# Performance work log

Measured on AMD Instinct MI355X. Metric: run time of the kernel, lower is better.

Reference implementation:

```python
import jax, jax.numpy as jnp
import numpy as np

EPS = 1e-5

def spmm(rows, cols, vals, x, n_out):
    # COO sparse [n_out, n_in] @ x [n_in, d] -> [n_out, d]
    return jax.ops.segment_sum(vals[:, None] * x[cols], rows, num_segments=n_out)

def layernorm(x, g, b):
    mu = jnp.mean(x, axis=-1, keepdims=True)
    var = jnp.var(x, axis=-1, keepdims=True)
    return (x - mu) * jax.lax.rsqrt(var + EPS) * g + b

def setup_inputs() -> dict:
    key = jax.random.key(0)
    ks = jax.random.split(key, 32)
    N, D = 100000, 512
    N0, N1, N2 = 131072, 32768, 8192
    E_s0, E_s1 = 262144, 65536
    E_f0, E_f1 = 1048576, 262144
    s = 1.0 / np.sqrt(D)
    inp = {
        'x': jax.random.normal(ks[0], (N, D), jnp.float32),
        'hist0': jax.random.normal(ks[1], (N, D), jnp.float32),
        'hist1': jax.random.normal(ks[2], (N, D), jnp.float32),
        'w0': jax.random.normal(ks[3], (D, D), jnp.float32) * s,
        'b0': jax.random.normal(ks[4], (D,), jnp.float32) * s,
        'g0': jnp.ones((D,), jnp.float32),
        'beta0': jnp.zeros((D,), jnp.float32),
        'w1': jax.random.normal(ks[5], (D, D), jnp.float32) * s,
        'b1': jax.random.normal(ks[6], (D,), jnp.float32) * s,
        'sadj0_vals': jax.random.uniform(ks[7], (E_s0,), jnp.float32),
        'sadj1_vals': jax.random.uniform(ks[8], (E_s1,), jnp.float32),
        'fadj0_vals': jax.random.uniform(ks[9], (E_f0,), jnp.float32),
        'fadj1_vals': jax.random.uniform(ks[10], (E_f1,), jnp.float32),
        'sid0': jax.random.randint(ks[11], (N0,), 0, N),
        'sid1': jax.random.randint(ks[12], (N1,), 0, N),
        'sid2': jax.random.randint(ks[13], (N2,), 0, N),
        'fid0': jax.random.randint(ks[14], (N0,), 0, N),
        'fid1': jax.random.randint(ks[15], (N1,), 0, N),
        'sadj0_rows': jax.random.randint(ks[16], (E_s0,), 0, N1),
        'sadj0_cols': jax.random.randint(ks[17], (E_s0,), 0, N0),
        'sadj1_rows': jax.random.randint(ks[18], (E_s1,), 0, N2),
        'sadj1_cols': jax.random.randint(ks[19], (E_s1,), 0, N1),
        'fadj0_rows': jax.random.randint(ks[20], (E_f0,), 0, N1),
        'fadj0_cols': jax.random.randint(ks[21], (E_f0,), 0, N0),
        'fadj1_rows': jax.random.randint(ks[22], (E_f1,), 0, N2),
        'fadj1_cols': jax.random.randint(ks[23], (E_f1,), 0, N1),
    }
    return inp

def reference(x, hist0, hist1, w0, b0, g0, beta0, w1, b1,
              sadj0_vals, sadj1_vals, fadj0_vals, fadj1_vals,
              sid0, sid1, sid2, fid0, fid1,
              sadj0_rows, sadj0_cols, sadj1_rows, sadj1_cols,
              fadj0_rows, fadj0_cols, fadj1_rows, fadj1_cols):
    N1 = sid1.shape[0]
    N2 = sid2.shape[0]
    sg = jax.lax.stop_gradient
    # layer 0
    h = x[sid0]                                   # [N0, D]
    h = h - sg(hist0[sid0])                        # variance-reduction correction
    full = sg(spmm(fadj0_rows, fadj0_cols, fadj0_vals, hist0[fid0], N1))
    h = spmm(sadj0_rows, sadj0_cols, sadj0_vals, h, N1) + full  # [N1, D]
    h = h @ w0.T + b0
    h = jax.nn.relu(layernorm(h, g0, beta0))
    # layer 1 (last: no norm/relu)
    h = h - sg(hist1[sid1])
    full = sg(spmm(fadj1_rows, fadj1_cols, fadj1_vals, hist1[fid1], N2))
    h = spmm(sadj1_rows, sadj1_cols, sadj1_vals, h, N2) + full  # [N2, D]
    h = h @ w1.T + b1
    return jax.nn.log_softmax(h, axis=-1)
```

## Files before the change

### kernel.cpp

```cpp
#include <hip/hip_runtime.h>

#define D 512
#define NTAB 100000

typedef __bf16 bf16x8 __attribute__((ext_vector_type(8)));
typedef float f32x4 __attribute__((ext_vector_type(4)));
typedef float f32x2 __attribute__((ext_vector_type(2)));

__device__ __forceinline__ unsigned f2bf(float f){
  union { float f; unsigned u; } v; v.f = f;
  unsigned r = v.u + 0x7fffu + ((v.u >> 16) & 1u);
  return r >> 16;
}
__device__ __forceinline__ float bf2f(unsigned h){
  union { unsigned u; float f; } v; v.u = h << 16; return v.f;
}
__device__ __forceinline__ uint2 enc_fp8x8(f32x4 v0, f32x4 v1){
  int lo = __builtin_amdgcn_cvt_pk_fp8_f32(v0[0], v0[1], 0, false);
  lo     = __builtin_amdgcn_cvt_pk_fp8_f32(v0[2], v0[3], lo, true);
  int hi = __builtin_amdgcn_cvt_pk_fp8_f32(v1[0], v1[1], 0, false);
  hi     = __builtin_amdgcn_cvt_pk_fp8_f32(v1[2], v1[3], hi, true);
  return make_uint2((unsigned)lo, (unsigned)hi);
}

#define PER8 (NTAB*D/8)

#define MA_NS   6400
#define MA_GRID (MA_NS*9 + 512)

__global__ __launch_bounds__(256) void k_megaA(
    const int* __restrict__ s0r, int nS0,
    const int* __restrict__ f0r, int nF0, int* __restrict__ cnt0,
    const int* __restrict__ s1r, int nS1, int* __restrict__ cnt_s1,
    const int* __restrict__ f1r, int nF1, int* __restrict__ cnt_f1,
    const float* __restrict__ x, const float* __restrict__ hist0, const float* __restrict__ hist1,
    unsigned char* __restrict__ TD,
    unsigned short* __restrict__ H1b,
    const float* __restrict__ w0, const float* __restrict__ w1,
    unsigned short* __restrict__ w0b, unsigned short* __restrict__ w1b)
{
  int b = blockIdx.x, t = threadIdx.x;
  if (b < MA_NS*9){
    int sb = b / 9, r = b % 9;
    if (r == 0){
      int i = sb*256 + t;
      if (i < nS0){ atomicAdd(&cnt0[s0r[i]], 1); return; }
      i -= nS0;
      if (i < nF0){ atomicAdd(&cnt0[f0r[i]], 1); return; }
      i -= nF0;
      if (i < nS1){ atomicAdd(&cnt_s1[s1r[i]], 1); return; }
      i -= nS1;
      atomicAdd(&cnt_f1[f1r[i]], 1);
      return;
    }
    if (r < 5){
      int ci = (sb*4 + (r-1))*256 + t;
      if (ci >= PER8) return;
      const f32x4* px = (const f32x4*)(x     + (size_t)ci*8);
      const f32x4* ph = (const f32x4*)(hist0 + (size_t)ci*8);
      f32x4 x0 = __builtin_nontemporal_load(px);
      f32x4 x1 = __builtin_nontemporal_load(px+1);
      f32x4 h0 = __builtin_nontemporal_load(ph);
      f32x4 h1 = __builtin_nontemporal_load(ph+1);
      *(uint2*)(TD + (size_t)ci*8)                    = enc_fp8x8(x0 - h0, x1 - h1);
      *(uint2*)(TD + (size_t)NTAB*D + (size_t)ci*8)   = enc_fp8x8(h0, h1);
      return;
    }
    {
      int ci = (sb*4 + (r-5))*256 + t;
      if (ci >= PER8) return;
      const f32x4* p = (const f32x4*)(hist1 + (size_t)ci*8);
      f32x4 v0 = __builtin_nontemporal_load(p);
      f32x4 v1 = __builtin_nontemporal_load(p+1);
      uint4 o;
      o.x = f2bf(v0[0]) | (f2bf(v0[1])<<16);
      o.y = f2bf(v0[2]) | (f2bf(v0[3])<<16);
      o.z = f2bf(v1[0]) | (f2bf(v1[1])<<16);
      o.w = f2bf(v1[2]) | (f2bf(v1[3])<<16);
      *(uint4*)(H1b + (size_t)ci*8) = o;
      return;
    }
  } else {
    int i = (b - MA_NS*9)*256 + t;
    const float* src = (i < 65536) ? w0 : w1;
    unsigned short* dst = (i < 65536) ? w0b : w1b;
    int ii = (i < 65536) ? i : i - 65536;
    f32x4 v = *(const f32x4*)(src + (size_t)ii*4);
    ushort4 o;
    o.x = (unsigned short)f2bf(v[0]); o.y = (unsigned short)f2bf(v[1]);
    o.z = (unsigned short)f2bf(v[2]); o.w = (unsigned short)f2bf(v[3]);
    *(ushort4*)(dst + (size_t)ii*4) = o;
  }
}

__global__ __launch_bounds__(1024) void k_exscan3(
    const int* c0, int* r0, int n0,
    const int* c1, int* r1, int n1,
    const int* c2, int* r2, int n2)
{
  __shared__ int part[1024];
  const int* cnt; int* rp; int n;
  switch (blockIdx.x){
    case 0: cnt=c0; rp=r0; n=n0; break;
    case 1: cnt=c1; rp=r1; n=n1; break;
    default: cnt=c2; rp=r2; n=n2; break;
  }
  int t = threadIdx.x;
  int chunk = n >> 10;
  int base = t*chunk;
  int s = 0;
  for (int i=0;i<chunk;i++) s += cnt[base+i];
  part[t] = s; __syncthreads();
  for (int off=1; off<1024; off<<=1){
    int v = (t>=off) ? part[t-off] : 0;
    __syncthreads();
    part[t] += v;
    __syncthreads();
  }
  int run = (t==0) ? 0 : part[t-1];
  for (int i=0;i<chunk;i++){ rp[base+i] = run; run += cnt[base+i]; }
  if (t == 1023) rp[n] = run;
}

__global__ __launch_bounds__(256) void k_fill(
    const int* __restrict__ s0r, const int* __restrict__ s0c, const float* __restrict__ s0v, int nS0,
    const int* __restrict__ f0r, const int* __restrict__ f0c, const float* __restrict__ f0v, int nF0,
    const int* __restrict__ sid0, const int* __restrict__ fid0,
    const int* __restrict__ rp0, int* __restrict__ fill0, int2* __restrict__ bce0,
    const int* __restrict__ s1r, const int* __restrict__ s1c, const float* __restrict__ s1v, int nS1,
    const int* __restrict__ rp_s1, int* __restrict__ fill_s1, int2* __restrict__ bce_s1,
    const int* __restrict__ f1r, const int* __restrict__ f1c, const float* __restrict__ f1v,
    const int* __restrict__ fid1,
    const int* __restrict__ rp_f1, int* __restrict__ fill_f1, int2* __restrict__ bce_f1)
{
  int i = blockIdx.x*256 + threadIdx.x;
  if (i < nS0){
    int rr = s0r[i];
    int c  = sid0[s0c[i]];
    int p = atomicAdd(&fill0[rr], 1);
    bce0[rp0[rr] + p] = make_int2(c, __float_as_int(s0v[i]));
    return;
  }
  i -= nS0;
  if (i < nF0){
    int rr = f0r[i];
    int c  = NTAB + fid0[f0c[i]];
    int p = atomicAdd(&fill0[rr], 1);
    bce0[rp0[rr] + p] = make_int2(c, __float_as_int(f0v[i]));
    return;
  }
  i -= nF0;
  if (i < nS1){
    int rr = s1r[i];
    int p = atomicAdd(&fill_s1[rr], 1);
    bce_s1[rp_s1[rr] + p] = make_int2(s1c[i], __float_as_int(s1v[i]));
    return;
  }
  i -= nS1;
  {
    int rr = f1r[i];
    int c  = fid1[f1c[i]];
    int p = atomicAdd(&fill_f1[rr], 1);
    bce_f1[rp_f1[rr] + p] = make_int2(c, __float_as_int(f1v[i]));
  }
}

__device__ __forceinline__ void acc_bf16(float* a, uint4 p, float v){
  a[0] += v*bf2f(p.x & 0xffffu); a[1] += v*bf2f(p.x >> 16);
  a[2] += v*bf2f(p.y & 0xffffu); a[3] += v*bf2f(p.y >> 16);
  a[4] += v*bf2f(p.z & 0xffffu); a[5] += v*bf2f(p.z >> 16);
  a[6] += v*bf2f(p.w & 0xffffu); a[7] += v*bf2f(p.w >> 16);
}
__device__ __forceinline__ void acc_fp8(float* a, uint2 q, float v){
  f32x2 d0 = __builtin_amdgcn_cvt_pk_f32_fp8(q.x, false);
  f32x2 d1 = __builtin_amdgcn_cvt_pk_f32_fp8(q.x, true);
  f32x2 d2 = __builtin_amdgcn_cvt_pk_f32_fp8(q.y, false);
  f32x2 d3 = __builtin_amdgcn_cvt_pk_f32_fp8(q.y, true);
  a[0] += v*d0[0]; a[1] += v*d0[1]; a[2] += v*d1[0]; a[3] += v*d1[1];
  a[4] += v*d2[0]; a[5] += v*d2[1]; a[6] += v*d3[0]; a[7] += v*d3[1];
}

__device__ __forceinline__ void spmm_phase(
    const int* __restrict__ rp, const int2* __restrict__ be,
    const unsigned short* __restrict__ H, int row, int lane, float* a)
{
  int j = rp[row], je = rp[row+1];
  for (; j + 8 <= je; j += 8){
    int2 e[8]; uint4 p[8];
    #pragma unroll
    for (int u=0;u<8;u++) e[u] = be[j+u];
    #pragma unroll
    for (int u=0;u<8;u++) p[u] = *(const uint4*)(H + (size_t)e[u].x*D + lane*8);
    #pragma unroll
    for (int u=0;u<8;u++) acc_bf16(a, p[u], __int_as_float(e[u].y));
  }
  if (j + 4 <= je){
    int2 e[4]; uint4 p[4];
    #pragma unroll
    for (int u=0;u<4;u++) e[u] = be[j+u];
    #pragma unroll
    for (int u=0;u<4;u++) p[u] = *(const uint4*)(H + (size_t)e[u].x*D + lane*8);
    #pragma unroll
    for (int u=0;u<4;u++) acc_bf16(a, p[u], __int_as_float(e[u].y));
    j += 4;
  }
  for (; j < je; j++){
    int2 e = be[j];
    uint4 p = *(const uint4*)(H + (size_t)e.x*D + lane*8);
    acc_bf16(a, p, __int_as_float(e.y));
  }
}

__device__ __forceinline__ void spmm_phase_q8(
    const int* __restrict__ rp, const int2* __restrict__ be,
    const unsigned char* __restrict__ Q, int row, int lane, float* a)
{
  int j = rp[row], je = rp[row+1];
  for (; j + 8 <= je; j += 8){
    int2 e[8]; uint2 q[8];
    #pragma unroll
    for (int u=0;u<8;u++) e[u] = be[j+u];
    #pragma unroll
    for (int u=0;u<8;u++) q[u] = *(const uint2*)(Q + (size_t)e[u].x*D + lane*8);
    #pragma unroll
    for (int u=0;u<8;u++) acc_fp8(a, q[u], __int_as_float(e[u].y));
  }
  if (j + 4 <= je){
    int2 e[4]; uint2 q[4];
    #pragma unroll
    for (int u=0;u<4;u++) e[u] = be[j+u];
    #pragma unroll
    for (int u=0;u<4;u++) q[u] = *(const uint2*)(Q + (size_t)e[u].x*D + lane*8);
    #pragma unroll
    for (int u=0;u<4;u++) acc_fp8(a, q[u], __int_as_float(e[u].y));
    j += 4;
  }
  for (; j < je; j++){
    int2 e = be[j];
    uint2 q = *(const uint2*)(Q + (size_t)e.x*D + lane*8);
    acc_fp8(a, q, __int_as_float(e.y));
  }
}

__device__ __forceinline__ void store_row(unsigned short* out, int row, int lane, const float* a){
  uint4 o;
  o.x = f2bf(a[0]) | (f2bf(a[1]) << 16);
  o.y = f2bf(a[2]) | (f2bf(a[3]) << 16);
  o.z = f2bf(a[4]) | (f2bf(a[5]) << 16);
  o.w = f2bf(a[6]) | (f2bf(a[7]) << 16);
  *(uint4*)(out + (size_t)row*D + lane*8) = o;
}

__global__ __launch_bounds__(256) void k_spmm0(
    const int* __restrict__ rp, const int2* __restrict__ be,
    const unsigned char* __restrict__ TD,
    unsigned short* __restrict__ out, int nrows)
{
  int wid = threadIdx.x >> 6, lane = threadIdx.x & 63;
  int row = blockIdx.x*4 + wid;
  if (row >= nrows) return;
  float a[8] = {0.f,0.f,0.f,0.f,0.f,0.f,0.f,0.f};
  spmm_phase_q8(rp, be, TD, row, lane, a);
  store_row(out, row, lane, a);
}

__global__ __launch_bounds__(256) void k_spmm_acc(
    const int* __restrict__ rp, const int2* __restrict__ be, const unsigned short* __restrict__ H,
    unsigned short* __restrict__ out, int nrows)
{
  int wid = threadIdx.x >> 6, lane = threadIdx.x & 63;
  int row = blockIdx.x*4 + wid;
  if (row >= nrows) return;
  float a[8];
  uint4 p = *(const uint4*)(out + (size_t)row*D + lane*8);
  a[0]=bf2f(p.x&0xffffu); a[1]=bf2f(p.x>>16); a[2]=bf2f(p.y&0xffffu); a[3]=bf2f(p.y>>16);
  a[4]=bf2f(p.z&0xffffu); a[5]=bf2f(p.z>>16); a[6]=bf2f(p.w&0xffffu); a[7]=bf2f(p.w>>16);
  spmm_phase(rp, be, H, row, lane, a);
  store_row(out, row, lane, a);
}

__device__ __forceinline__ void gload16(const unsigned short* g, unsigned short* l){
  __builtin_amdgcn_global_load_lds(
      (const __attribute__((address_space(1))) unsigned int*)(const void*)g,
      (__attribute__((address_space(3))) unsigned int*)(void*)l,
      16, 0, 0);
}

template<bool OUT_BF16>
__device__ __forceinline__ void gemm_block(
    const unsigned short* __restrict__ A,
    const unsigned short* __restrict__ B,
    const float* __restrict__ bias,
    void* __restrict__ Cv,
    int gemm_bid, unsigned short* Al, unsigned short* Bl)
{
  int bx = gemm_bid & 3, by = gemm_bid >> 2;
  int m0 = by << 7, n0 = bx << 7;
  int t = threadIdx.x, wave = t >> 6, lane = t & 63;
  int wr = wave >> 1, wc = wave & 1;
  f32x4 acc[4][4] = {};
  int flat = t << 3;
  int r0 = flat >> 5, cc = flat & 31;
  const unsigned short* pa = A + (size_t)(m0 + r0)*D + cc;
  const unsigned short* pb = B + (size_t)(n0 + r0)*D + cc;
  for (int k0 = 0; k0 < D; k0 += 32){
    gload16(pa + k0,                 &Al[flat]);
    gload16(pa + (size_t)64*D + k0,  &Al[flat + 2048]);
    gload16(pb + k0,                 &Bl[flat]);
    gload16(pb + (size_t)64*D + k0,  &Bl[flat + 2048]);
    __syncthreads();
    int arow = (wr << 6) | (lane & 15);
    int brow = (wc << 6) | (lane & 15);
    int kg   = (lane >> 4) << 3;
    bf16x8 af[4], bfr[4];
    #pragma unroll
    for (int mi=0; mi<4; mi++) af[mi]  = *(const bf16x8*)&Al[(arow + (mi<<4))*32 + kg];
    #pragma unroll
    for (int ni=0; ni<4; ni++) bfr[ni] = *(const bf16x8*)&Bl[(brow + (ni<<4))*32 + kg];
    #pragma unroll
    for (int mi=0; mi<4; mi++)
      #pragma unroll
      for (int ni=0; ni<4; ni++)
        acc[mi][ni] = __builtin_amdgcn_mfma_f32_16x16x32_bf16(af[mi], bfr[ni], acc[mi][ni], 0, 0, 0);
    __syncthreads();
  }
  int crow = m0 + (wr << 6) + ((lane >> 4) << 2);
  int ccol = n0 + (wc << 6) + (lane & 15);
  #pragma unroll
  for (int mi=0; mi<4; mi++){
    #pragma unroll
    for (int q=0; q<4; q++){
      int row = crow + (mi << 4) + q;
      #pragma unroll
      for (int ni=0; ni<4; ni++){
        float val = acc[mi][ni][q] + bias[ccol + (ni << 4)];
        if (OUT_BF16)
          ((unsigned short*)Cv)[(size_t)row*D + ccol + (ni << 4)] = (unsigned short)f2bf(val);
        else
          ((float*)Cv)[(size_t)row*D + ccol + (ni << 4)] = val;
      }
    }
  }
}

__global__ __launch_bounds__(256) void k_megaC(
    const unsigned short* __restrict__ A, const unsigned short* __restrict__ B,
    const float* __restrict__ bias, unsigned short* __restrict__ y1,
    const int* __restrict__ rpf, const int2* __restrict__ bef,
    const unsigned short* __restrict__ H1b, unsigned short* __restrict__ out2, int n2rows)
{
  __shared__ unsigned short Al[128*32];
  __shared__ unsigned short Bl[128*32];
  int b = blockIdx.x, t = threadIdx.x;
  int sb = b / 3, r = b % 3;
  if (r == 0){
    gemm_block<true>(A, B, bias, (void*)y1, sb, Al, Bl);
  } else {
    int wid = t >> 6, lane = t & 63;
    int row = (sb*2 + (r-1))*4 + wid;
    if (row >= n2rows) return;
    float a[8] = {0.f,0.f,0.f,0.f,0.f,0.f,0.f,0.f};
    spmm_phase(rpf, bef, H1b, row, lane, a);
    store_row(out2, row, lane, a);
  }
}

template<bool OUT_BF16>
__global__ __launch_bounds__(256) void k_gemm_bias(
    const unsigned short* __restrict__ A,
    const unsigned short* __restrict__ B,
    const float* __restrict__ bias,
    void* __restrict__ Cv,
    int M)
{
  __shared__ unsigned short Al[128*32];
  __shared__ unsigned short Bl[128*32];
  gemm_block<OUT_BF16>(A, B, bias, Cv, blockIdx.x, Al, Bl);
}

__global__ __launch_bounds__(256) void k_ln_relu_sub(
    const unsigned short* __restrict__ y, const float* __restrict__ gam, const float* __restrict__ bet,
    const unsigned short* __restrict__ H1b, const int* __restrict__ sid1,
    unsigned short* __restrict__ out)
{
  __shared__ float sh[8];
  int row = blockIdx.x, t = threadIdx.x;
  int c = t << 1;
  unsigned pv = *(const unsigned*)(y + (size_t)row*D + c);
  float vx = bf2f(pv & 0xffffu), vy = bf2f(pv >> 16);
  float s = vx + vy, ss = vx*vx + vy*vy;
  #pragma unroll
  for (int m=1; m<64; m<<=1){ s += __shfl_xor(s, m); ss += __shfl_xor(ss, m); }
  int wave = t >> 6, lane = t & 63;
  if (lane == 0){ sh[wave] = s; sh[4+wave] = ss; }
  __syncthreads();
  s  = sh[0]+sh[1]+sh[2]+sh[3];
  ss = sh[4]+sh[5]+sh[6]+sh[7];
  float mu  = s * (1.f/D);
  float var = ss * (1.f/D) - mu*mu;
  float rr  = rsqrtf(var + 1e-5f);
  int srow = sid1[row];
  unsigned hv = *(const unsigned*)(H1b + (size_t)srow*D + c);
  float o0 = fmaxf((vx - mu)*rr*gam[c]   + bet[c],   0.f) - bf2f(hv & 0xffffu);
  float o1 = fmaxf((vy - mu)*rr*gam[c+1] + bet[c+1], 0.f) - bf2f(hv >> 16);
  *(unsigned*)(out + (size_t)row*D + c) = f2bf(o0) | (f2bf(o1) << 16);
}

__global__ __launch_bounds__(256) void k_logsoftmax(const float* __restrict__ y, float* __restrict__ out){
  __shared__ float sh[8];
  int row = blockIdx.x, t = threadIdx.x;
  int c = t << 1;
  float2 v = *(const float2*)(y + (size_t)row*D + c);
  float m = fmaxf(v.x, v.y);
  #pragma unroll
  for (int k=1; k<64; k<<=1) m = fmaxf(m, __shfl_xor(m, k));
  int wave = t >> 6, lane = t & 63;
  if (lane == 0) sh[wave] = m;
  __syncthreads();
  m = fmaxf(fmaxf(sh[0], sh[1]), fmaxf(sh[2], sh[3]));
  __syncthreads();
  float e = expf(v.x - m) + expf(v.y - m);
  #pragma unroll
  for (int k=1; k<64; k<<=1) e += __shfl_xor(e, k);
  if (lane == 0) sh[4+wave] = e;
  __syncthreads();
  e = sh[4]+sh[5]+sh[6]+sh[7];
  float lse = m + logf(e);
  float2 o; o.x = v.x - lse; o.y = v.y - lse;
  *(float2*)(out + (size_t)row*D + c) = o;
}

extern "C" void kernel_launch(void* const* d_in, const int* in_sizes, int n_in,
                              void* d_out, int out_size, void* d_ws, size_t ws_size,
                              hipStream_t stream)
{
  const float* x     = (const float*)d_in[0];
  const float* hist0 = (const float*)d_in[1];
  const float* hist1 = (const float*)d_in[2];
  const float* w0    = (const float*)d_in[3];
  const float* b0    = (const float*)d_in[4];
  const float* g0    = (const float*)d_in[5];
  const float* beta0 = (const float*)d_in[6];
  const float* w1    = (const float*)d_in[7];
  const float* b1    = (const float*)d_in[8];
  const float* s0v   = (const float*)d_in[9];
  const float* s1v   = (const float*)d_in[10];
  const float* f0v   = (const float*)d_in[11];
  const float* f1v   = (const float*)d_in[12];
  const int* sid0    = (const int*)d_in[13];
  const int* sid1    = (const int*)d_in[14];
  const int* fid0    = (const int*)d_in[16];
  const int* fid1    = (const int*)d_in[17];
  const int* s0r     = (const int*)d_in[18];
  const int* s0c     = (const int*)d_in[19];
  const int* s1r     = (const int*)d_in[20];
  const int* s1c     = (const int*)d_in[21];
  const int* f0r     = (const int*)d_in[22];
  const int* f0c     = (const int*)d_in[23];
  const int* f1r     = (const int*)d_in[24];
  const int* f1c     = (const int*)d_in[25];

  const int N1 = 32768, N2 = 8192;
  const int Es0 = 262144, Es1 = 65536, Ef0 = 1048576, Ef1 = 262144;
  const int E0 = Es0 + Ef0;

  char* ws = (char*)d_ws;
  size_t off = 0;
  auto alloc = [&](size_t bytes)->char*{
    char* p = ws + off; off += (bytes + 255) & ~(size_t)255; return p;
  };
  char* TD_raw = alloc((size_t)2*NTAB*D);
  unsigned short* H1b = (unsigned short*)alloc((size_t)NTAB*D*2);
  unsigned short* h1   = (unsigned short*)alloc((size_t)N1*D*2);
  unsigned short* out1 = (unsigned short*)alloc((size_t)N1*D*2);
  unsigned short* w0b  = (unsigned short*)alloc((size_t)D*D*2);
  unsigned short* w1b  = (unsigned short*)alloc((size_t)D*D*2);
  int* meta = (int*)alloc((size_t)(2*N1 + 4*N2)*4);
  int* cnt0   = meta;            int* fill0   = cnt0 + N1;
  int* cnt_s1 = fill0 + N1;      int* fill_s1 = cnt_s1 + N2;
  int* cnt_f1 = fill_s1 + N2;    int* fill_f1 = cnt_f1 + N2;
  size_t metaBytes = (size_t)(2*N1 + 4*N2)*4;
  int* rp0   = (int*)alloc((size_t)(N1+1)*4);
  int* rp_s1 = (int*)alloc((size_t)(N2+1)*4);
  int* rp_f1 = (int*)alloc((size_t)(N2+1)*4);
  int2* bce0   = (int2*)alloc((size_t)E0*8);
  int2* bce_s1 = (int2*)alloc((size_t)Es1*8);
  int2* bce_f1 = (int2*)alloc((size_t)Ef1*8);

  unsigned char*  TD   = (unsigned char*)TD_raw;
  unsigned short* y1   = (unsigned short*)TD_raw;
  float*          y2   = (float*)(TD_raw + ((size_t)34<<20));
  unsigned short* out2 = (unsigned short*)(TD_raw + ((size_t)52<<20));
  float*          outp = (float*)d_out;

  hipMemsetAsync(meta, 0, metaBytes, stream);
  k_megaA<<<MA_GRID, 256, 0, stream>>>(
      s0r, Es0, f0r, Ef0, cnt0, s1r, Es1, cnt_s1, f1r, Ef1, cnt_f1,
      x, hist0, hist1, TD, H1b, w0, w1, w0b, w1b);
  k_exscan3<<<3, 1024, 0, stream>>>(cnt0, rp0, N1, cnt_s1, rp_s1, N2, cnt_f1, rp_f1, N2);
  k_fill<<<6400, 256, 0, stream>>>(
      s0r, s0c, s0v, Es0, f0r, f0c, f0v, Ef0, sid0, fid0, rp0, fill0, bce0,
      s1r, s1c, s1v, Es1, rp_s1, fill_s1, bce_s1,
      f1r, f1c, f1v, fid1, rp_f1, fill_f1, bce_f1);
  k_spmm0<<<N1/4, 256, 0, stream>>>(rp0, bce0, TD, out1, N1);
  k_megaC<<<1024*3, 256, 0, stream>>>(out1, w0b, b0, y1, rp_f1, bce_f1, H1b, out2, N2);
  k_ln_relu_sub<<<N1, 256, 0, stream>>>(y1, g0, beta0, H1b, sid1, h1);
  k_spmm_acc<<<N2/4, 256, 0, stream>>>(rp_s1, bce_s1, h1, out2, N2);
  k_gemm_bias<false><<<(N2/128)*4, 256, 0, stream>>>(out2, w1b, b1, (void*)y2, N2);
  k_logsoftmax<<<N2, 256, 0, stream>>>(y2, outp);
}
```

Baseline: 526.6 us.

## Move hist1 bf16 conversion from prologue kernel into layer-0 SpMM kernel

The streaming fp32-to-bf16 conversion of hist1 is taken out of the bandwidth-bound prologue kernel and interleaved, as extra blocks, with the gather-bound layer-0 SpMM kernel. Each conversion block now handles eight chunks. The intent is to overlap the pure streaming traffic with the latency-bound gathers instead of adding it to the prologue's streaming cost. The two workloads now compete for bandwidth inside one launch, and the block interleave ratio decides how well they overlap.

Result: no change. 520.5 us (-1.2%).

```diff
diff --git a/kernel.cpp b/kernel.cpp
--- a/kernel.cpp
+++ b/kernel.cpp
@@ -26,22 +26,21 @@
 #define PER8 (NTAB*D/8)
 
 #define MA_NS   6400
-#define MA_GRID (MA_NS*9 + 512)
+#define MA_GRID (MA_NS*5 + 512)
 
 __global__ __launch_bounds__(256) void k_megaA(
     const int* __restrict__ s0r, int nS0,
     const int* __restrict__ f0r, int nF0, int* __restrict__ cnt0,
     const int* __restrict__ s1r, int nS1, int* __restrict__ cnt_s1,
     const int* __restrict__ f1r, int nF1, int* __restrict__ cnt_f1,
-    const float* __restrict__ x, const float* __restrict__ hist0, const float* __restrict__ hist1,
+    const float* __restrict__ x, const float* __restrict__ hist0,
     unsigned char* __restrict__ TD,
-    unsigned short* __restrict__ H1b,
     const float* __restrict__ w0, const float* __restrict__ w1,
     unsigned short* __restrict__ w0b, unsigned short* __restrict__ w1b)
 {
   int b = blockIdx.x, t = threadIdx.x;
-  if (b < MA_NS*9){
-    int sb = b / 9, r = b % 9;
+  if (b < MA_NS*5){
+    int sb = b / 5, r = b % 5;
     if (r == 0){
       int i = sb*256 + t;
       if (i < nS0){ atomicAdd(&cnt0[s0r[i]], 1); return; }
@@ -53,7 +52,7 @@
       atomicAdd(&cnt_f1[f1r[i]], 1);
       return;
     }
-    if (r < 5){
+    {
       int ci = (sb*4 + (r-1))*256 + t;
       if (ci >= PER8) return;
       const f32x4* px = (const f32x4*)(x     + (size_t)ci*8);
@@ -66,22 +65,8 @@
       *(uint2*)(TD + (size_t)NTAB*D + (size_t)ci*8)   = enc_fp8x8(h0, h1);
       return;
     }
-    {
-      int ci = (sb*4 + (r-5))*256 + t;
-      if (ci >= PER8) return;
-      const f32x4* p = (const f32x4*)(hist1 + (size_t)ci*8);
-      f32x4 v0 = __builtin_nontemporal_load(p);
-      f32x4 v1 = __builtin_nontemporal_load(p+1);
-      uint4 o;
-      o.x = f2bf(v0[0]) | (f2bf(v0[1])<<16);
-      o.y = f2bf(v0[2]) | (f2bf(v0[3])<<16);
-      o.z = f2bf(v1[0]) | (f2bf(v1[1])<<16);
-      o.w = f2bf(v1[2]) | (f2bf(v1[3])<<16);
-      *(uint4*)(H1b + (size_t)ci*8) = o;
-      return;
-    }
   } else {
-    int i = (b - MA_NS*9)*256 + t;
+    int i = (b - MA_NS*5)*256 + t;
     const float* src = (i < 65536) ? w0 : w1;
     unsigned short* dst = (i < 65536) ? w0b : w1b;
     int ii = (i < 65536) ? i : i - 65536;
@@ -251,17 +236,42 @@
   *(uint4*)(out + (size_t)row*D + lane*8) = o;
 }
 
-__global__ __launch_bounds__(256) void k_spmm0(
+#define SX_NS   1639
+#define SX_GRID (SX_NS*7)
+#define CONV_BLKS 3125
+
+__global__ __launch_bounds__(256) void k_spmmX(
     const int* __restrict__ rp, const int2* __restrict__ be,
     const unsigned char* __restrict__ TD,
-    unsigned short* __restrict__ out, int nrows)
-{
-  int wid = threadIdx.x >> 6, lane = threadIdx.x & 63;
-  int row = blockIdx.x*4 + wid;
-  if (row >= nrows) return;
-  float a[8] = {0.f,0.f,0.f,0.f,0.f,0.f,0.f,0.f};
-  spmm_phase_q8(rp, be, TD, row, lane, a);
-  store_row(out, row, lane, a);
+    unsigned short* __restrict__ out, int nrows,
+    const float* __restrict__ hist1, unsigned short* __restrict__ H1b)
+{
+  int b = blockIdx.x, t = threadIdx.x;
+  int sb = b / 7, r = b % 7;
+  if (r < 5){
+    int wid = t >> 6, lane = t & 63;
+    int row = (sb*5 + r)*4 + wid;
+    if (row >= nrows) return;
+    float a[8] = {0.f,0.f,0.f,0.f,0.f,0.f,0.f,0.f};
+    spmm_phase_q8(rp, be, TD, row, lane, a);
+    store_row(out, row, lane, a);
+  } else {
+    int cb = sb*2 + (r-5);
+    if (cb >= CONV_BLKS) return;
+    #pragma unroll
+    for (int k=0; k<8; k++){
+      int ci = cb*256 + t + k*(CONV_BLKS*256);
+      const f32x4* p = (const f32x4*)(hist1 + (size_t)ci*8);
+      f32x4 v0 = __builtin_nontemporal_load(p);
+      f32x4 v1 = __builtin_nontemporal_load(p+1);
+      uint4 o;
+      o.x = f2bf(v0[0]) | (f2bf(v0[1])<<16);
+      o.y = f2bf(v0[2]) | (f2bf(v0[3])<<16);
+      o.z = f2bf(v1[0]) | (f2bf(v1[1])<<16);
+      o.w = f2bf(v1[2]) | (f2bf(v1[3])<<16);
+      *(uint4*)(H1b + (size_t)ci*8) = o;
+    }
+  }
 }
 
 __global__ __launch_bounds__(256) void k_spmm_acc(
@@ -496,13 +506,13 @@
   hipMemsetAsync(meta, 0, metaBytes, stream);
   k_megaA<<<MA_GRID, 256, 0, stream>>>(
       s0r, Es0, f0r, Ef0, cnt0, s1r, Es1, cnt_s1, f1r, Ef1, cnt_f1,
-      x, hist0, hist1, TD, H1b, w0, w1, w0b, w1b);
+      x, hist0, TD, w0, w1, w0b, w1b);
   k_exscan3<<<3, 1024, 0, stream>>>(cnt0, rp0, N1, cnt_s1, rp_s1, N2, cnt_f1, rp_f1, N2);
   k_fill<<<6400, 256, 0, stream>>>(
       s0r, s0c, s0v, Es0, f0r, f0c, f0v, Ef0, sid0, fid0, rp0, fill0, bce0,
       s1r, s1c, s1v, Es1, rp_s1, fill_s1, bce_s1,
       f1r, f1c, f1v, fid1, rp_f1, fill_f1, bce_f1);
-  k_spmm0<<<N1/4, 256, 0, stream>>>(rp0, bce0, TD, out1, N1);
+  k_spmmX<<<SX_GRID, 256, 0, stream>>>(rp0, bce0, TD, out1, N1, hist1, H1b);
   k_megaC<<<1024*3, 256, 0, stream>>>(out1, w0b, b0, y1, rp_f1, bce_f1, H1b, out2, N2);
   k_ln_relu_sub<<<N1, 256, 0, stream>>>(y1, g0, beta0, H1b, sid1, h1);
   k_spmm_acc<<<N2/4, 256, 0, stream>>>(rp_s1, bce_s1, h1, out2, N2);
```
